# Performance work log

Hardware: AMD Instinct MI355X
Metric: run time of the kernel (lower is better)

Reference implementation:

```python
import jax, jax.numpy as jnp
import numpy as np

EPS_LN = 1e-5
EPS_STD = 1e-5


def _ln_dim1(z, g, b):
    # LayerNorm over channel dim (axis=1) of (B, C, T) or (B, C, 1)
    mu = z.mean(axis=1, keepdims=True)
    var = ((z - mu) ** 2).mean(axis=1, keepdims=True)
    return (z - mu) * jax.lax.rsqrt(var + EPS_LN) * g[None, :, None] + b[None, :, None]


def _stats(x, m):
    # weighted mean/std over time axis; m broadcasts over channels
    mean = (m * x).sum(axis=2)                                   # (B, C)
    std = jnp.sqrt(jnp.maximum((m * x * x).sum(axis=2) - mean ** 2, EPS_STD))
    return mean, std


def setup_inputs() -> dict:
    key = jax.random.key(0)
    ks = jax.random.split(key, 4)
    B, C, T, H = 16, 1536, 2000, 128
    x = jax.random.normal(ks[0], (B, C, T), dtype=jnp.float32)
    mask = jnp.ones((B, 1, T), dtype=jnp.float32)
    # attention MLP params (conv1x1 -> relu -> LN(dim=1) -> tanh -> conv1x1)
    w1 = jax.random.normal(ks[1], (H, 3 * C), dtype=jnp.float32) * (1.0 / np.sqrt(3 * C))
    b1 = jnp.zeros((H,), jnp.float32)
    g1 = jnp.ones((H,), jnp.float32)
    be1 = jnp.zeros((H,), jnp.float32)
    w2 = jax.random.normal(ks[2], (C, H), dtype=jnp.float32) * (1.0 / np.sqrt(H))
    b2 = jnp.zeros((C,), jnp.float32)
    g2 = jnp.ones((2 * C,), jnp.float32)
    be2 = jnp.zeros((2 * C,), jnp.float32)
    return {"x": x, "mask": mask, "w1": w1, "b1": b1, "g1": g1, "be1": be1,
            "w2": w2, "b2": b2, "g2": g2, "be2": be2}


def reference(x, mask, w1, b1, g1, be1, w2, b2, g2, be2):
    B, C, T = x.shape
    # time_attention: append masked global mean/std, broadcast over T
    total = mask.sum(axis=2, keepdims=True)                      # (B,1,1)
    mean0, std0 = _stats(x, mask / total)                        # (B,C)
    x_in = jnp.concatenate([
        x,
        jnp.broadcast_to(mean0[:, :, None], (B, C, T)),
        jnp.broadcast_to(std0[:, :, None], (B, C, T)),
    ], axis=1)                                                   # (B,3C,T)
    # attention MLP (conv1x1 == channel matmul)
    h = jnp.einsum("hc,bct->bht", w1, x_in) + b1[None, :, None]  # (B,H,T)
    h = jnp.tanh(_ln_dim1(jax.nn.relu(h), g1, be1))
    alpha = jnp.einsum("ch,bht->bct", w2, h) + b2[None, :, None]  # (B,C,T)
    # masked softmax over time
    alpha = jnp.where(mask == 0, -jnp.inf, alpha)
    alpha = jax.nn.softmax(alpha, axis=2)
    # attention-weighted stats
    mean, std = _stats(x, alpha)                                 # (B,C) each
    out = jnp.concatenate([mean, std], axis=1)[:, :, None]       # (B,2C,1)
    return _ln_dim1(out, g2, be2)
```

## Files before the change

kernel.cpp:

```cpp
#include <hip/hip_runtime.h>
#include <math.h>

constexpr int B_  = 16;
constexpr int C_  = 1536;
constexpr int T_  = 2000;
constexpr int H_  = 128;
constexpr int C3_ = 3 * C_;
constexpr int C2_ = 2 * C_;
constexpr int NT_ = 4;

typedef short bf8 __attribute__((ext_vector_type(8)));
typedef short bf4 __attribute__((ext_vector_type(4)));
typedef float f4  __attribute__((ext_vector_type(4)));

__device__ inline unsigned short f2b(float f) {
  unsigned int u = __builtin_bit_cast(unsigned int, f);
  unsigned int r = (u + 0x7FFFu + ((u >> 16) & 1u)) >> 16;
  return (unsigned short)r;
}

__global__ __launch_bounds__(256) void k_stats(
    const float* __restrict__ x, const float* __restrict__ mask,
    float* __restrict__ mean0, float* __restrict__ std0) {
  const int wave = threadIdx.x >> 6;
  const int lane = threadIdx.x & 63;
  const int row = blockIdx.x * 4 + wave;
  const int b = row / C_;
  const float4* xr = (const float4*)(x + (size_t)row * T_);
  const float4* mr = (const float4*)(mask + (size_t)b * T_);
  float sm = 0.f, s1 = 0.f, s2 = 0.f;
  for (int i = lane; i < T_ / 4; i += 64) {
    float4 xv = xr[i];
    float4 mv = mr[i];
    sm += mv.x + mv.y + mv.z + mv.w;
    s1 += mv.x * xv.x + mv.y * xv.y + mv.z * xv.z + mv.w * xv.w;
    s2 += mv.x * xv.x * xv.x + mv.y * xv.y * xv.y + mv.z * xv.z * xv.z + mv.w * xv.w * xv.w;
  }
#pragma unroll
  for (int off = 32; off; off >>= 1) {
    sm += __shfl_xor(sm, off);
    s1 += __shfl_xor(s1, off);
    s2 += __shfl_xor(s2, off);
  }
  if (lane == 0) {
    float mean = s1 / sm;
    float var = s2 / sm - mean * mean;
    mean0[row] = mean;
    std0[row] = sqrtf(fmaxf(var, 1e-5f));
  }
}

__global__ __launch_bounds__(256) void k_hconst_wl1(
    const float* __restrict__ w1, const float* __restrict__ b1,
    const float* __restrict__ mean0, const float* __restrict__ std0,
    const float* __restrict__ w2,
    float* __restrict__ hconst, float* __restrict__ wl1) {
  const int wave = threadIdx.x >> 6;
  const int lane = threadIdx.x & 63;
  if (blockIdx.x < B_ * H_ / 4) {
    const int idx = blockIdx.x * 4 + wave;
    const int b = idx >> 7;
    const int h = idx & (H_ - 1);
    const float* wm  = w1 + (size_t)h * C3_ + C_;
    const float* wsd = wm + C_;
    const float* mn = mean0 + b * C_;
    const float* sd = std0 + b * C_;
    float s = 0.f;
    for (int c = lane; c < C_; c += 64)
      s += wm[c] * mn[c] + wsd[c] * sd[c];
#pragma unroll
    for (int off = 32; off; off >>= 1) s += __shfl_xor(s, off);
    if (lane == 0) hconst[idx] = s + b1[h];
  } else {
    const int c = (blockIdx.x - B_ * H_ / 4) * 4 + wave;
    const float* wr = w2 + (size_t)c * H_;
    float s = fabsf(wr[lane]) + fabsf(wr[lane + 64]);
#pragma unroll
    for (int off = 32; off; off >>= 1) s += __shfl_xor(s, off);
    if (lane == 0) wl1[c] = s;
  }
}

__global__ __launch_bounds__(256) void k_gemm1_ln(
    const float* __restrict__ x, const float* __restrict__ w1,
    const float* __restrict__ hconst, const float* __restrict__ g1,
    const float* __restrict__ be1, unsigned short* __restrict__ hlnT) {
  __shared__ __align__(16) short As[2][128 * 32];
  __shared__ __align__(16) short Bs[2][64 * 32];
  const int b = blockIdx.y;
  const int t0 = blockIdx.x * 64;
  const int tid = threadIdx.x;
  const int lane = tid & 63;
  const int w = tid >> 6;
  const int l15 = lane & 15;
  const int l4 = lane >> 4;

  float4 va[4], vb[2];

  f4 acc[8];
#pragma unroll
  for (int mi = 0; mi < 8; ++mi) { f4 z = {0.f, 0.f, 0.f, 0.f}; acc[mi] = z; }

#define G1_GLOAD(K0)                                                          \
  {                                                                           \
    _Pragma("unroll")                                                         \
    for (int q = 0; q < 4; ++q) {                                             \
      int idx = q * 256 + tid;                                                \
      int row = idx >> 3, j4 = idx & 7;                                       \
      va[q] = *(const float4*)(w1 + (size_t)row * C3_ + (K0) + j4 * 4);       \
    }                                                                         \
    _Pragma("unroll")                                                         \
    for (int q = 0; q < 2; ++q) {                                             \
      int idx = q * 256 + tid;                                                \
      int k = idx >> 4, t4 = idx & 15;                                        \
      int t = t0 + t4 * 4;                                                    \
      if (t < T_)                                                             \
        vb[q] = *(const float4*)(x + ((size_t)(b * C_ + (K0) + k)) * T_ + t); \
      else                                                                    \
        vb[q] = make_float4(0.f, 0.f, 0.f, 0.f);                              \
    }                                                                         \
  }
#define G1_LSTORE(BUF)                                                        \
  {                                                                           \
    _Pragma("unroll")                                                         \
    for (int q = 0; q < 4; ++q) {                                             \
      int idx = q * 256 + tid;                                                \
      int row = idx >> 3, j4 = idx & 7;                                       \
      int slot = (j4 >> 1) ^ ((row >> 2) & 3);                                \
      bf4 p;                                                                  \
      p[0] = (short)f2b(va[q].x); p[1] = (short)f2b(va[q].y);                 \
      p[2] = (short)f2b(va[q].z); p[3] = (short)f2b(va[q].w);                 \
      *(bf4*)&As[BUF][row * 32 + slot * 8 + (j4 & 1) * 4] = p;                \
    }                                                                         \
    _Pragma("unroll")                                                         \
    for (int q = 0; q < 2; ++q) {                                             \
      int idx = q * 256 + tid;                                                \
      int k = idx >> 4, t4 = idx & 15;                                        \
      float vv[4] = {vb[q].x, vb[q].y, vb[q].z, vb[q].w};                     \
      _Pragma("unroll")                                                       \
      for (int j = 0; j < 4; ++j) {                                           \
        int row = t4 * 4 + j;                                                 \
        int slot = (k >> 3) ^ ((row >> 2) & 3);                               \
        Bs[BUF][row * 32 + slot * 8 + (k & 7)] = (short)f2b(vv[j]);           \
      }                                                                       \
    }                                                                         \
  }

  G1_GLOAD(0);
  G1_LSTORE(0);
  __syncthreads();

  const int fA = (l15 >> 2) & 3;
  const int NS = C_ / 32;
  for (int s = 0; s < NS; ++s) {
    const int cur = s & 1;
    if (s + 1 < NS) G1_GLOAD((s + 1) * 32);
    {
      const int browB = w * 16 + l15;
      bf8 bfr = *(const bf8*)&Bs[cur][browB * 32 + (l4 ^ fA) * 8];
#pragma unroll
      for (int mi = 0; mi < 8; ++mi) {
        bf8 afr = *(const bf8*)&As[cur][(mi * 16 + l15) * 32 + (l4 ^ fA) * 8];
        acc[mi] = __builtin_amdgcn_mfma_f32_16x16x32_bf16(afr, bfr, acc[mi], 0, 0, 0);
      }
    }
    if (s + 1 < NS) G1_LSTORE(cur ^ 1);
    __syncthreads();
  }

  const int t = t0 + w * 16 + l15;
  float sum = 0.f, ssq = 0.f;
#pragma unroll
  for (int mi = 0; mi < 8; ++mi) {
    float4 h4 = *(const float4*)(hconst + b * H_ + mi * 16 + l4 * 4);
    const float* hp = (const float*)&h4;
#pragma unroll
    for (int reg = 0; reg < 4; ++reg) {
      float v = fmaxf(acc[mi][reg] + hp[reg], 0.f);
      acc[mi][reg] = v;
      sum += v;
      ssq += v * v;
    }
  }
  sum += __shfl_xor(sum, 16); sum += __shfl_xor(sum, 32);
  ssq += __shfl_xor(ssq, 16); ssq += __shfl_xor(ssq, 32);
  const float mean = sum * (1.f / 128.f);
  const float rstd = rsqrtf(ssq * (1.f / 128.f) - mean * mean + 1e-5f);
  if (t < T_) {
    unsigned short* dst = hlnT + ((size_t)b * T_ + t) * H_;
#pragma unroll
    for (int mi = 0; mi < 8; ++mi) {
      float4 g4 = *(const float4*)(g1 + mi * 16 + l4 * 4);
      float4 e4 = *(const float4*)(be1 + mi * 16 + l4 * 4);
      const float* gp = (const float*)&g4;
      const float* ep = (const float*)&e4;
      bf4 p;
#pragma unroll
      for (int reg = 0; reg < 4; ++reg) {
        float o = tanhf((acc[mi][reg] - mean) * rstd * gp[reg] + ep[reg]);
        p[reg] = (short)f2b(o);
      }
      *(bf4*)&dst[mi * 16 + l4 * 4] = p;
    }
  }
}

__global__ __launch_bounds__(256) void k_gemm2_pool(
    const float* __restrict__ x, const float* __restrict__ mask,
    const float* __restrict__ w2, const unsigned short* __restrict__ hlnT,
    const float* __restrict__ wl1,
    float* __restrict__ ps0, float* __restrict__ ps1, float* __restrict__ ps2) {
  __shared__ __align__(16) short Hs[2][64 * 128];
  const int b = blockIdx.y;
  const int c0 = blockIdx.x * 128;
  const int part = blockIdx.z;
  const int tb = part * 512;
  const int te = min(tb + 512, T_);
  const int tid = threadIdx.x;
  const int lane = tid & 63;
  const int w = tid >> 6;
  const int l15 = lane & 15;
  const int l4 = lane >> 4;

  bf8 af[2][4];
#pragma unroll
  for (int mi = 0; mi < 2; ++mi)
#pragma unroll
    for (int ks = 0; ks < 4; ++ks) {
      const float* src = w2 + (size_t)(c0 + w * 32 + mi * 16 + l15) * H_ + (ks * 4 + l4) * 8;
      float4 v0 = *(const float4*)src;
      float4 v1 = *(const float4*)(src + 4);
      bf8 p;
      p[0] = (short)f2b(v0.x); p[1] = (short)f2b(v0.y);
      p[2] = (short)f2b(v0.z); p[3] = (short)f2b(v0.w);
      p[4] = (short)f2b(v1.x); p[5] = (short)f2b(v1.y);
      p[6] = (short)f2b(v1.z); p[7] = (short)f2b(v1.w);
      af[mi][ks] = p;
    }

  float Mc[8];
#pragma unroll
  for (int mi = 0; mi < 2; ++mi) {
    float4 m4 = *(const float4*)(wl1 + c0 + w * 32 + mi * 16 + l4 * 4);
    Mc[mi * 4 + 0] = m4.x; Mc[mi * 4 + 1] = m4.y;
    Mc[mi * 4 + 2] = m4.z; Mc[mi * 4 + 3] = m4.w;
  }

  float s0[8], s1[8], s2[8];
#pragma unroll
  for (int r = 0; r < 8; ++r) { s0[r] = 0.f; s1[r] = 0.f; s2[r] = 0.f; }

  bf8 hreg[4];
#define G2_HLOAD(T0)                                                          \
  {                                                                           \
    _Pragma("unroll")                                                         \
    for (int q = 0; q < 4; ++q) {                                             \
      int idx = q * 256 + tid;                                                \
      int row = idx >> 4, slot = idx & 15;                                    \
      int t = (T0) + row;                                                     \
      if (t > T_ - 1) t = T_ - 1;                                             \
      hreg[q] = *(const bf8*)(hlnT + ((size_t)b * T_ + t) * H_ + slot * 8);   \
    }                                                                         \
  }
#define G2_HSTORE(BUF)                                                        \
  {                                                                           \
    _Pragma("unroll")                                                         \
    for (int q = 0; q < 4; ++q) {                                             \
      int idx = q * 256 + tid;                                                \
      int row = idx >> 4, slot = idx & 15;                                    \
      *(bf8*)&Hs[BUF][row * 128 + (slot ^ (row & 15)) * 8] = hreg[q];         \
    }                                                                         \
  }

  G2_HLOAD(tb);
  G2_HSTORE(0);
  __syncthreads();

  const int NCH = (te - tb + 63) / 64;
  for (int ch = 0; ch < NCH; ++ch) {
    const int t0 = tb + ch * 64;
    const int cur = ch & 1;
    if (ch + 1 < NCH) G2_HLOAD(t0 + 64);

    float mk[4];
    int tcol[4];
#pragma unroll
    for (int nj = 0; nj < 4; ++nj) {
      int t = t0 + nj * 16 + l15;
      tcol[nj] = (t < T_) ? t : (T_ - 1);
      mk[nj] = (t < T_) ? mask[(size_t)b * T_ + t] : 0.f;
    }
    float xv[8][4];
#pragma unroll
    for (int mi = 0; mi < 2; ++mi)
#pragma unroll
      for (int reg = 0; reg < 4; ++reg) {
        const int c = c0 + w * 32 + mi * 16 + l4 * 4 + reg;
        const float* xrow = x + ((size_t)(b * C_ + c)) * T_;
#pragma unroll
        for (int nj = 0; nj < 4; ++nj) xv[mi * 4 + reg][nj] = xrow[tcol[nj]];
      }

    f4 acc[2][4];
#pragma unroll
    for (int mi = 0; mi < 2; ++mi)
#pragma unroll
      for (int nj = 0; nj < 4; ++nj) { f4 z = {0.f, 0.f, 0.f, 0.f}; acc[mi][nj] = z; }

#pragma unroll
    for (int ks = 0; ks < 4; ++ks) {
      const int sw = (ks * 4 + l4) ^ l15;
      bf8 bb[4];
#pragma unroll
      for (int nj = 0; nj < 4; ++nj)
        bb[nj] = *(const bf8*)&Hs[cur][(nj * 16 + l15) * 128 + sw * 8];
#pragma unroll
      for (int nj = 0; nj < 4; ++nj) {
        acc[0][nj] = __builtin_amdgcn_mfma_f32_16x16x32_bf16(af[0][ks], bb[nj], acc[0][nj], 0, 0, 0);
        acc[1][nj] = __builtin_amdgcn_mfma_f32_16x16x32_bf16(af[1][ks], bb[nj], acc[1][nj], 0, 0, 0);
      }
    }

#pragma unroll
    for (int mi = 0; mi < 2; ++mi)
#pragma unroll
      for (int reg = 0; reg < 4; ++reg) {
        const int r = mi * 4 + reg;
        float a0 = s0[r], a1 = s1[r], a2 = s2[r];
#pragma unroll
        for (int nj = 0; nj < 4; ++nj) {
          float e = (mk[nj] != 0.f) ? __expf(acc[mi][nj][reg] - Mc[r]) : 0.f;
          float xvv = xv[r][nj];
          a0 += e; a1 += e * xvv; a2 += e * xvv * xvv;
        }
        s0[r] = a0; s1[r] = a1; s2[r] = a2;
      }

    if (ch + 1 < NCH) G2_HSTORE(cur ^ 1);
    __syncthreads();
  }

#pragma unroll
  for (int off = 1; off < 16; off <<= 1) {
#pragma unroll
    for (int r = 0; r < 8; ++r) {
      s0[r] += __shfl_xor(s0[r], off);
      s1[r] += __shfl_xor(s1[r], off);
      s2[r] += __shfl_xor(s2[r], off);
    }
  }
  if (l15 == 0) {
#pragma unroll
    for (int mi = 0; mi < 2; ++mi)
#pragma unroll
      for (int reg = 0; reg < 4; ++reg) {
        const int r = mi * 4 + reg;
        const int c = c0 + w * 32 + mi * 16 + l4 * 4 + reg;
        const size_t j = ((size_t)(b * NT_ + part)) * C_ + c;
        ps0[j] = s0[r]; ps1[j] = s1[r]; ps2[j] = s2[r];
      }
  }
}

__global__ __launch_bounds__(256) void k_pool_merge(
    const float* __restrict__ ps0, const float* __restrict__ ps1,
    const float* __restrict__ ps2, float* __restrict__ pooled) {
  const int idx = blockIdx.x * 256 + threadIdx.x;
  const int b = idx / C_;
  const int c = idx - b * C_;
  float s0 = 0.f, s1 = 0.f, s2 = 0.f;
#pragma unroll
  for (int p = 0; p < NT_; ++p) {
    const size_t j = ((size_t)(b * NT_ + p)) * C_ + c;
    s0 += ps0[j]; s1 += ps1[j]; s2 += ps2[j];
  }
  float mean = s1 / s0;
  float var = s2 / s0 - mean * mean;
  pooled[b * C2_ + c] = mean;
  pooled[b * C2_ + C_ + c] = sqrtf(fmaxf(var, 1e-5f));
}

__global__ __launch_bounds__(256) void k_final_ln(
    const float* __restrict__ pooled, const float* __restrict__ g2,
    const float* __restrict__ be2, float* __restrict__ out) {
  __shared__ float rs[8];
  const int b = blockIdx.x;
  const int tid = threadIdx.x;
  const int lane = tid & 63;
  const int wave = tid >> 6;
  const float* p = pooled + b * C2_;
  float s = 0.f, q = 0.f;
  for (int i = tid; i < C2_; i += 256) {
    float v = p[i];
    s += v;
    q += v * v;
  }
#pragma unroll
  for (int off = 32; off; off >>= 1) {
    s += __shfl_xor(s, off);
    q += __shfl_xor(q, off);
  }
  if (lane == 0) { rs[wave] = s; rs[4 + wave] = q; }
  __syncthreads();
  s = rs[0] + rs[1] + rs[2] + rs[3];
  q = rs[4] + rs[5] + rs[6] + rs[7];
  float mean = s * (1.f / C2_);
  float var = q * (1.f / C2_) - mean * mean;
  float rstd = rsqrtf(var + 1e-5f);
  for (int i = tid; i < C2_; i += 256)
    out[b * C2_ + i] = (p[i] - mean) * rstd * g2[i] + be2[i];
}

extern "C" void kernel_launch(void* const* d_in, const int* in_sizes, int n_in,
                              void* d_out, int out_size, void* d_ws, size_t ws_size,
                              hipStream_t stream) {
  const float* x    = (const float*)d_in[0];
  const float* mask = (const float*)d_in[1];
  const float* w1   = (const float*)d_in[2];
  const float* b1   = (const float*)d_in[3];
  const float* g1   = (const float*)d_in[4];
  const float* be1  = (const float*)d_in[5];
  const float* w2   = (const float*)d_in[6];
  const float* g2   = (const float*)d_in[8];
  const float* be2  = (const float*)d_in[9];
  float* out = (float*)d_out;

  float* ws     = (float*)d_ws;
  float* mean0  = ws;
  float* std0   = mean0 + B_ * C_;
  float* hconst = std0 + B_ * C_;
  float* pooled = hconst + B_ * H_;
  float* wl1    = pooled + B_ * C2_;
  float* ps0    = wl1 + C_;
  float* ps1    = ps0 + B_ * NT_ * C_;
  float* ps2    = ps1 + B_ * NT_ * C_;
  unsigned short* hlnT = (unsigned short*)(ps2 + B_ * NT_ * C_);

  k_stats<<<dim3(B_ * C_ / 4), dim3(256), 0, stream>>>(x, mask, mean0, std0);
  k_hconst_wl1<<<dim3(B_ * H_ / 4 + C_ / 4), dim3(256), 0, stream>>>(
      w1, b1, mean0, std0, w2, hconst, wl1);
  k_gemm1_ln<<<dim3((T_ + 63) / 64, B_), dim3(256), 0, stream>>>(x, w1, hconst, g1, be1, hlnT);
  k_gemm2_pool<<<dim3(C_ / 128, B_, NT_), dim3(256), 0, stream>>>(x, mask, w2, hlnT, wl1,
                                                                  ps0, ps1, ps2);
  k_pool_merge<<<dim3(B_ * C_ / 256), dim3(256), 0, stream>>>(ps0, ps1, ps2, pooled);
  k_final_ln<<<dim3(B_), dim3(256), 0, stream>>>(pooled, g2, be2, out);
}
```

Before: 164.2 us.

## Fuse masked mean/std statistics pass into GEMM1 and split off LayerNorm epilogue

The standalone statistics kernel that re-read all of x is removed. Per-tile masked sums of x and x^2 are now computed inside the first GEMM while its x tiles are loaded, and a small reduce kernel merges them. Because hconst depends on those stats, GEMM1 writes the pre-activation h to an fp32 buffer, and a separate epilogue kernel adds hconst and applies relu, LayerNorm and tanh. This saves one full pass over x (about 200 MB) at the cost of an extra h_pre round trip (about 16 MB), partial-sum buffers and one more kernel launch.

```diff
diff --git a/kernel.cpp b/kernel.cpp
--- a/kernel.cpp
+++ b/kernel.cpp
@@ -8,6 +8,7 @@
 constexpr int C3_ = 3 * C_;
 constexpr int C2_ = 2 * C_;
 constexpr int NT_ = 4;
+constexpr int NTL_ = 32;
 
 typedef short bf8 __attribute__((ext_vector_type(8)));
 typedef short bf4 __attribute__((ext_vector_type(4)));
@@ -19,35 +20,171 @@
   return (unsigned short)r;
 }
 
-__global__ __launch_bounds__(256) void k_stats(
-    const float* __restrict__ x, const float* __restrict__ mask,
+__global__ __launch_bounds__(256) void k_gemm1_stats(
+    const float* __restrict__ x, const float* __restrict__ w1,
+    const float* __restrict__ mask,
+    float* __restrict__ h_pre, float* __restrict__ sp1, float* __restrict__ sp2) {
+  __shared__ __align__(16) short As[2][128 * 32];
+  __shared__ __align__(16) short Bs[2][64 * 32];
+  const int b = blockIdx.y;
+  const int tile = blockIdx.x;
+  const int t0 = tile * 64;
+  const int tid = threadIdx.x;
+  const int lane = tid & 63;
+  const int w = tid >> 6;
+  const int l15 = lane & 15;
+  const int l4 = lane >> 4;
+
+  float4 va[4], vb[2];
+
+  const int t4 = tid & 15;
+  float mreg[4];
+#pragma unroll
+  for (int j = 0; j < 4; ++j) {
+    int t = t0 + t4 * 4 + j;
+    mreg[j] = (t < T_) ? mask[(size_t)b * T_ + t] : 0.f;
+  }
+  float* sp1row = sp1 + ((size_t)b * NTL_ + tile) * C_;
+  float* sp2row = sp2 + ((size_t)b * NTL_ + tile) * C_;
+
+  f4 acc[8];
+#pragma unroll
+  for (int mi = 0; mi < 8; ++mi) { f4 z = {0.f, 0.f, 0.f, 0.f}; acc[mi] = z; }
+
+#define G1_GLOAD(K0)                                                          \
+  {                                                                           \
+    _Pragma("unroll")                                                         \
+    for (int q = 0; q < 4; ++q) {                                             \
+      int idx = q * 256 + tid;                                                \
+      int row = idx >> 3, j4 = idx & 7;                                       \
+      va[q] = *(const float4*)(w1 + (size_t)row * C3_ + (K0) + j4 * 4);       \
+    }                                                                         \
+    _Pragma("unroll")                                                         \
+    for (int q = 0; q < 2; ++q) {                                             \
+      int idx = q * 256 + tid;                                                \
+      int k = idx >> 4;                                                       \
+      int t = t0 + t4 * 4;                                                    \
+      if (t < T_)                                                             \
+        vb[q] = *(const float4*)(x + ((size_t)(b * C_ + (K0) + k)) * T_ + t); \
+      else                                                                    \
+        vb[q] = make_float4(0.f, 0.f, 0.f, 0.f);                              \
+    }                                                                         \
+  }
+#define G1_LSTORE(BUF)                                                        \
+  {                                                                           \
+    _Pragma("unroll")                                                         \
+    for (int q = 0; q < 4; ++q) {                                             \
+      int idx = q * 256 + tid;                                                \
+      int row = idx >> 3, j4 = idx & 7;                                       \
+      int slot = (j4 >> 1) ^ ((row >> 2) & 3);                                \
+      bf4 p;                                                                  \
+      p[0] = (short)f2b(va[q].x); p[1] = (short)f2b(va[q].y);                 \
+      p[2] = (short)f2b(va[q].z); p[3] = (short)f2b(va[q].w);                 \
+      *(bf4*)&As[BUF][row * 32 + slot * 8 + (j4 & 1) * 4] = p;                \
+    }                                                                         \
+    _Pragma("unroll")                                                         \
+    for (int q = 0; q < 2; ++q) {                                             \
+      int idx = q * 256 + tid;                                                \
+      int k = idx >> 4;                                                       \
+      float vv[4] = {vb[q].x, vb[q].y, vb[q].z, vb[q].w};                     \
+      _Pragma("unroll")                                                       \
+      for (int j = 0; j < 4; ++j) {                                           \
+        int row = t4 * 4 + j;                                                 \
+        int slot = (k >> 3) ^ ((row >> 2) & 3);                               \
+        Bs[BUF][row * 32 + slot * 8 + (k & 7)] = (short)f2b(vv[j]);           \
+      }                                                                       \
+    }                                                                         \
+  }
+#define G1_STATS(K0)                                                          \
+  {                                                                           \
+    _Pragma("unroll")                                                         \
+    for (int q = 0; q < 2; ++q) {                                             \
+      float vv[4] = {vb[q].x, vb[q].y, vb[q].z, vb[q].w};                     \
+      float a1 = 0.f, a2 = 0.f;                                               \
+      _Pragma("unroll")                                                       \
+      for (int j = 0; j < 4; ++j) {                                           \
+        float mx = mreg[j] * vv[j];                                           \
+        a1 += mx;                                                             \
+        a2 = fmaf(mx, vv[j], a2);                                             \
+      }                                                                       \
+      _Pragma("unroll")                                                       \
+      for (int off = 1; off < 16; off <<= 1) {                                \
+        a1 += __shfl_xor(a1, off);                                            \
+        a2 += __shfl_xor(a2, off);                                            \
+      }                                                                       \
+      if (t4 == 0) {                                                          \
+        int c = (K0) + q * 16 + (tid >> 4);                                   \
+        sp1row[c] = a1;                                                       \
+        sp2row[c] = a2;                                                       \
+      }                                                                       \
+    }                                                                         \
+  }
+
+  G1_GLOAD(0);
+  G1_LSTORE(0);
+  G1_STATS(0);
+  __syncthreads();
+
+  const int fA = (l15 >> 2) & 3;
+  const int NS = C_ / 32;
+  for (int s = 0; s < NS; ++s) {
+    const int cur = s & 1;
+    if (s + 1 < NS) G1_GLOAD((s + 1) * 32);
+    {
+      const int browB = w * 16 + l15;
+      bf8 bfr = *(const bf8*)&Bs[cur][browB * 32 + (l4 ^ fA) * 8];
+#pragma unroll
+      for (int mi = 0; mi < 8; ++mi) {
+        bf8 afr = *(const bf8*)&As[cur][(mi * 16 + l15) * 32 + (l4 ^ fA) * 8];
+        acc[mi] = __builtin_amdgcn_mfma_f32_16x16x32_bf16(afr, bfr, acc[mi], 0, 0, 0);
+      }
+    }
+    if (s + 1 < NS) {
+      G1_LSTORE(cur ^ 1);
+      G1_STATS((s + 1) * 32);
+    }
+    __syncthreads();
+  }
+
+  const int t = t0 + w * 16 + l15;
+  if (t < T_) {
+    float* dst = h_pre + ((size_t)b * T_ + t) * H_;
+#pragma unroll
+    for (int mi = 0; mi < 8; ++mi)
+      *(f4*)&dst[mi * 16 + l4 * 4] = acc[mi];
+  }
+}
+
+__global__ __launch_bounds__(256) void k_stats_reduce(
+    const float* __restrict__ sp1, const float* __restrict__ sp2,
+    const float* __restrict__ mask,
     float* __restrict__ mean0, float* __restrict__ std0) {
-  const int wave = threadIdx.x >> 6;
-  const int lane = threadIdx.x & 63;
-  const int row = blockIdx.x * 4 + wave;
-  const int b = row / C_;
-  const float4* xr = (const float4*)(x + (size_t)row * T_);
-  const float4* mr = (const float4*)(mask + (size_t)b * T_);
-  float sm = 0.f, s1 = 0.f, s2 = 0.f;
-  for (int i = lane; i < T_ / 4; i += 64) {
-    float4 xv = xr[i];
-    float4 mv = mr[i];
-    sm += mv.x + mv.y + mv.z + mv.w;
-    s1 += mv.x * xv.x + mv.y * xv.y + mv.z * xv.z + mv.w * xv.w;
-    s2 += mv.x * xv.x * xv.x + mv.y * xv.y * xv.y + mv.z * xv.z * xv.z + mv.w * xv.w * xv.w;
-  }
-#pragma unroll
-  for (int off = 32; off; off >>= 1) {
-    sm += __shfl_xor(sm, off);
-    s1 += __shfl_xor(s1, off);
-    s2 += __shfl_xor(s2, off);
-  }
-  if (lane == 0) {
-    float mean = s1 / sm;
-    float var = s2 / sm - mean * mean;
-    mean0[row] = mean;
-    std0[row] = sqrtf(fmaxf(var, 1e-5f));
-  }
+  __shared__ float rs[4];
+  const int b = blockIdx.x / (C_ / 256);
+  const int chunk = blockIdx.x % (C_ / 256);
+  const int tid = threadIdx.x;
+  const int lane = tid & 63;
+  const int wv = tid >> 6;
+  float sm = 0.f;
+  for (int i = tid; i < T_; i += 256) sm += mask[(size_t)b * T_ + i];
+#pragma unroll
+  for (int off = 32; off; off >>= 1) sm += __shfl_xor(sm, off);
+  if (lane == 0) rs[wv] = sm;
+  __syncthreads();
+  sm = rs[0] + rs[1] + rs[2] + rs[3];
+
+  const int c = chunk * 256 + tid;
+  float s1 = 0.f, s2 = 0.f;
+#pragma unroll 8
+  for (int tile = 0; tile < NTL_; ++tile) {
+    const size_t j = ((size_t)b * NTL_ + tile) * C_ + c;
+    s1 += sp1[j];
+    s2 += sp2[j];
+  }
+  float mean = s1 / sm;
+  float var = s2 / sm - mean * mean;
+  mean0[b * C_ + c] = mean;
+  std0[b * C_ + c] = sqrtf(fmaxf(var, 1e-5f));
 }
 
 __global__ __launch_bounds__(256) void k_hconst_wl1(
@@ -81,127 +218,48 @@
   }
 }
 
-__global__ __launch_bounds__(256) void k_gemm1_ln(
-    const float* __restrict__ x, const float* __restrict__ w1,
-    const float* __restrict__ hconst, const float* __restrict__ g1,
-    const float* __restrict__ be1, unsigned short* __restrict__ hlnT) {
-  __shared__ __align__(16) short As[2][128 * 32];
-  __shared__ __align__(16) short Bs[2][64 * 32];
+__global__ __launch_bounds__(256) void k_ln_epi(
+    const float* __restrict__ h_pre, const float* __restrict__ hconst,
+    const float* __restrict__ g1, const float* __restrict__ be1,
+    unsigned short* __restrict__ hlnT) {
   const int b = blockIdx.y;
-  const int t0 = blockIdx.x * 64;
-  const int tid = threadIdx.x;
-  const int lane = tid & 63;
-  const int w = tid >> 6;
-  const int l15 = lane & 15;
-  const int l4 = lane >> 4;
-
-  float4 va[4], vb[2];
-
-  f4 acc[8];
-#pragma unroll
-  for (int mi = 0; mi < 8; ++mi) { f4 z = {0.f, 0.f, 0.f, 0.f}; acc[mi] = z; }
-
-#define G1_GLOAD(K0)                                                          \
-  {                                                                           \
-    _Pragma("unroll")                                                         \
-    for (int q = 0; q < 4; ++q) {                                             \
-      int idx = q * 256 + tid;                                                \
-      int row = idx >> 3, j4 = idx & 7;                                       \
-      va[q] = *(const float4*)(w1 + (size_t)row * C3_ + (K0) + j4 * 4);       \
-    }                                                                         \
-    _Pragma("unroll")                                                         \
-    for (int q = 0; q < 2; ++q) {                                             \
-      int idx = q * 256 + tid;                                                \
-      int k = idx >> 4, t4 = idx & 15;                                        \
-      int t = t0 + t4 * 4;                                                    \
-      if (t < T_)                                                             \
-        vb[q] = *(const float4*)(x + ((size_t)(b * C_ + (K0) + k)) * T_ + t); \
-      else                                                                    \
-        vb[q] = make_float4(0.f, 0.f, 0.f, 0.f);                              \
-    }                                                                         \
-  }
-#define G1_LSTORE(BUF)                                                        \
-  {                                                                           \
-    _Pragma("unroll")                                                         \
-    for (int q = 0; q < 4; ++q) {                                             \
-      int idx = q * 256 + tid;                                                \
-      int row = idx >> 3, j4 = idx & 7;                                       \
-      int slot = (j4 >> 1) ^ ((row >> 2) & 3);                                \
-      bf4 p;                                                                  \
-      p[0] = (short)f2b(va[q].x); p[1] = (short)f2b(va[q].y);                 \
-      p[2] = (short)f2b(va[q].z); p[3] = (short)f2b(va[q].w);                 \
-      *(bf4*)&As[BUF][row * 32 + slot * 8 + (j4 & 1) * 4] = p;                \
-    }                                                                         \
-    _Pragma("unroll")                                                         \
-    for (int q = 0; q < 2; ++q) {                                             \
-      int idx = q * 256 + tid;                                                \
-      int k = idx >> 4, t4 = idx & 15;                                        \
-      float vv[4] = {vb[q].x, vb[q].y, vb[q].z, vb[q].w};                     \
-      _Pragma("unroll")                                                       \
-      for (int j = 0; j < 4; ++j) {                                           \
-        int row = t4 * 4 + j;                                                 \
-        int slot = (k >> 3) ^ ((row >> 2) & 3);                               \
-        Bs[BUF][row * 32 + slot * 8 + (k & 7)] = (short)f2b(vv[j]);           \
-      }                                                                       \
-    }                                                                         \
-  }
-
-  G1_GLOAD(0);
-  G1_LSTORE(0);
-  __syncthreads();
-
-  const int fA = (l15 >> 2) & 3;
-  const int NS = C_ / 32;
-  for (int s = 0; s < NS; ++s) {
-    const int cur = s & 1;
-    if (s + 1 < NS) G1_GLOAD((s + 1) * 32);
-    {
-      const int browB = w * 16 + l15;
-      bf8 bfr = *(const bf8*)&Bs[cur][browB * 32 + (l4 ^ fA) * 8];
-#pragma unroll
-      for (int mi = 0; mi < 8; ++mi) {
-        bf8 afr = *(const bf8*)&As[cur][(mi * 16 + l15) * 32 + (l4 ^ fA) * 8];
-        acc[mi] = __builtin_amdgcn_mfma_f32_16x16x32_bf16(afr, bfr, acc[mi], 0, 0, 0);
-      }
-    }
-    if (s + 1 < NS) G1_LSTORE(cur ^ 1);
-    __syncthreads();
-  }
-
-  const int t = t0 + w * 16 + l15;
+  const int t = blockIdx.x * 64 + (threadIdx.x >> 2);
+  const int part = threadIdx.x & 3;
+  if (t >= T_) return;
+  const float* src = h_pre + ((size_t)b * T_ + t) * H_ + part * 32;
+  const float* hc = hconst + b * H_ + part * 32;
+  float v[32];
   float sum = 0.f, ssq = 0.f;
 #pragma unroll
-  for (int mi = 0; mi < 8; ++mi) {
-    float4 h4 = *(const float4*)(hconst + b * H_ + mi * 16 + l4 * 4);
+  for (int j = 0; j < 8; ++j) {
+    float4 h4 = *(const float4*)(src + j * 4);
+    float4 c4 = *(const float4*)(hc + j * 4);
     const float* hp = (const float*)&h4;
-#pragma unroll
-    for (int reg = 0; reg < 4; ++reg) {
-      float v = fmaxf(acc[mi][reg] + hp[reg], 0.f);
-      acc[mi][reg] = v;
-      sum += v;
-      ssq += v * v;
-    }
-  }
-  sum += __shfl_xor(sum, 16); sum += __shfl_xor(sum, 32);
-  ssq += __shfl_xor(ssq, 16); ssq += __shfl_xor(ssq, 32);
+    const float* cp = (const float*)&c4;
+#pragma unroll
+    for (int r = 0; r < 4; ++r) {
+      float u = fmaxf(hp[r] + cp[r], 0.f);
+      v[j * 4 + r] = u;
+      sum += u;
+      ssq += u * u;
+    }
+  }
+  sum += __shfl_xor(sum, 1); sum += __shfl_xor(sum, 2);
+  ssq += __shfl_xor(ssq, 1); ssq += __shfl_xor(ssq, 2);
   const float mean = sum * (1.f / 128.f);
   const float rstd = rsqrtf(ssq * (1.f / 128.f) - mean * mean + 1e-5f);
-  if (t < T_) {
-    unsigned short* dst = hlnT + ((size_t)b * T_ + t) * H_;
-#pragma unroll
-    for (int mi = 0; mi < 8; ++mi) {
-      float4 g4 = *(const float4*)(g1 + mi * 16 + l4 * 4);
-      float4 e4 = *(const float4*)(be1 + mi * 16 + l4 * 4);
-      const float* gp = (const float*)&g4;
-      const float* ep = (const float*)&e4;
-      bf4 p;
-#pragma unroll
-      for (int reg = 0; reg < 4; ++reg) {
-        float o = tanhf((acc[mi][reg] - mean) * rstd * gp[reg] + ep[reg]);
-        p[reg] = (short)f2b(o);
-      }
-      *(bf4*)&dst[mi * 16 + l4 * 4] = p;
-    }
+  unsigned short* dst = hlnT + ((size_t)b * T_ + t) * H_ + part * 32;
+  const float* gp = g1 + part * 32;
+  const float* ep = be1 + part * 32;
+#pragma unroll
+  for (int m = 0; m < 4; ++m) {
+    bf8 p;
+#pragma unroll
+    for (int r = 0; r < 8; ++r) {
+      int j = m * 8 + r;
+      p[r] = (short)f2b(tanhf((v[j] - mean) * rstd * gp[j] + ep[j]));
+    }
+    *(bf8*)&dst[m * 8] = p;
   }
 }
 
@@ -434,12 +492,16 @@
   float* ps0    = wl1 + C_;
   float* ps1    = ps0 + B_ * NT_ * C_;
   float* ps2    = ps1 + B_ * NT_ * C_;
-  unsigned short* hlnT = (unsigned short*)(ps2 + B_ * NT_ * C_);
-
-  k_stats<<<dim3(B_ * C_ / 4), dim3(256), 0, stream>>>(x, mask, mean0, std0);
+  float* sp1    = ps2 + B_ * NT_ * C_;
+  float* sp2    = sp1 + B_ * NTL_ * C_;
+  float* h_pre  = sp2 + B_ * NTL_ * C_;
+  unsigned short* hlnT = (unsigned short*)(h_pre + (size_t)B_ * T_ * H_);
+
+  k_gemm1_stats<<<dim3(NTL_, B_), dim3(256), 0, stream>>>(x, w1, mask, h_pre, sp1, sp2);
+  k_stats_reduce<<<dim3(B_ * C_ / 256), dim3(256), 0, stream>>>(sp1, sp2, mask, mean0, std0);
   k_hconst_wl1<<<dim3(B_ * H_ / 4 + C_ / 4), dim3(256), 0, stream>>>(
       w1, b1, mean0, std0, w2, hconst, wl1);
-  k_gemm1_ln<<<dim3((T_ + 63) / 64, B_), dim3(256), 0, stream>>>(x, w1, hconst, g1, be1, hlnT);
+  k_ln_epi<<<dim3(NTL_, B_), dim3(256), 0, stream>>>(h_pre, hconst, g1, be1, hlnT);
   k_gemm2_pool<<<dim3(C_ / 128, B_, NT_), dim3(256), 0, stream>>>(x, mask, w2, hlnT, wl1,
                                                                   ps0, ps1, ps2);
   k_pool_merge<<<dim3(B_ * C_ / 256), dim3(256), 0, stream>>>(ps0, ps1, ps2, pooled);
```

After: 163.8 us. No clear change (-0.2%).

## Load x fragments directly into registers in gemm1, halve gemm2 channel tile

Applied to the files above, without the earlier changes.

In the first GEMM, the x operand is no longer staged through shared memory. Each lane loads its own 8 strided x values per k-step straight into registers, with a two-register ping-pong, and converts them to bf16 for the MFMA B fragment. This drops the Bs LDS buffer and its scattered 2-byte stores. The pooling GEMM now uses 64-channel blocks instead of 128, which doubles the grid and cuts per-thread registers. The bf16 conversion now uses the compiler's native __bf16 cast. The tradeoff is uncoalesced-looking global loads, since each lane reads 8 rows with stride T, though lanes in a row are contiguous in t.

```diff
diff --git a/kernel.cpp b/kernel.cpp
--- a/kernel.cpp
+++ b/kernel.cpp
@@ -1,4 +1,5 @@
 #include <hip/hip_runtime.h>
+#include <hip/hip_bf16.h>
 #include <math.h>
 
 constexpr int B_  = 16;
@@ -14,9 +15,8 @@
 typedef float f4  __attribute__((ext_vector_type(4)));
 
 __device__ inline unsigned short f2b(float f) {
-  unsigned int u = __builtin_bit_cast(unsigned int, f);
-  unsigned int r = (u + 0x7FFFu + ((u >> 16) & 1u)) >> 16;
-  return (unsigned short)r;
+  __bf16 h = (__bf16)f;
+  return __builtin_bit_cast(unsigned short, h);
 }
 
 __global__ __launch_bounds__(256) void k_stats(
@@ -86,7 +86,6 @@
     const float* __restrict__ hconst, const float* __restrict__ g1,
     const float* __restrict__ be1, unsigned short* __restrict__ hlnT) {
   __shared__ __align__(16) short As[2][128 * 32];
-  __shared__ __align__(16) short Bs[2][64 * 32];
   const int b = blockIdx.y;
   const int t0 = blockIdx.x * 64;
   const int tid = threadIdx.x;
@@ -94,14 +93,17 @@
   const int w = tid >> 6;
   const int l15 = lane & 15;
   const int l4 = lane >> 4;
-
-  float4 va[4], vb[2];
+  const int tcl = min(t0 + w * 16 + l15, T_ - 1);
+  const float* xcol = x + (size_t)b * C_ * T_ + tcl;
+
+  float4 va[4];
+  float xs0[8], xs1[8];
 
   f4 acc[8];
 #pragma unroll
   for (int mi = 0; mi < 8; ++mi) { f4 z = {0.f, 0.f, 0.f, 0.f}; acc[mi] = z; }
 
-#define G1_GLOAD(K0)                                                          \
+#define G1_GLOADA(K0)                                                         \
   {                                                                           \
     _Pragma("unroll")                                                         \
     for (int q = 0; q < 4; ++q) {                                             \
@@ -109,18 +111,14 @@
       int row = idx >> 3, j4 = idx & 7;                                       \
       va[q] = *(const float4*)(w1 + (size_t)row * C3_ + (K0) + j4 * 4);       \
     }                                                                         \
-    _Pragma("unroll")                                                         \
-    for (int q = 0; q < 2; ++q) {                                             \
-      int idx = q * 256 + tid;                                                \
-      int k = idx >> 4, t4 = idx & 15;                                        \
-      int t = t0 + t4 * 4;                                                    \
-      if (t < T_)                                                             \
-        vb[q] = *(const float4*)(x + ((size_t)(b * C_ + (K0) + k)) * T_ + t); \
-      else                                                                    \
-        vb[q] = make_float4(0.f, 0.f, 0.f, 0.f);                              \
-    }                                                                         \
-  }
-#define G1_LSTORE(BUF)                                                        \
+  }
+#define G1_GLOADB(K0, XS)                                                     \
+  {                                                                           \
+    const float* xb = xcol + ((size_t)(K0) + l4 * 8) * T_;                    \
+    _Pragma("unroll")                                                         \
+    for (int j = 0; j < 8; ++j) XS[j] = xb[(size_t)j * T_];                   \
+  }
+#define G1_LSTOREA(BUF)                                                       \
   {                                                                           \
     _Pragma("unroll")                                                         \
     for (int q = 0; q < 4; ++q) {                                             \
@@ -132,40 +130,36 @@
       p[2] = (short)f2b(va[q].z); p[3] = (short)f2b(va[q].w);                 \
       *(bf4*)&As[BUF][row * 32 + slot * 8 + (j4 & 1) * 4] = p;                \
     }                                                                         \
-    _Pragma("unroll")                                                         \
-    for (int q = 0; q < 2; ++q) {                                             \
-      int idx = q * 256 + tid;                                                \
-      int k = idx >> 4, t4 = idx & 15;                                        \
-      float vv[4] = {vb[q].x, vb[q].y, vb[q].z, vb[q].w};                     \
-      _Pragma("unroll")                                                       \
-      for (int j = 0; j < 4; ++j) {                                           \
-        int row = t4 * 4 + j;                                                 \
-        int slot = (k >> 3) ^ ((row >> 2) & 3);                               \
-        Bs[BUF][row * 32 + slot * 8 + (k & 7)] = (short)f2b(vv[j]);           \
-      }                                                                       \
-    }                                                                         \
-  }
-
-  G1_GLOAD(0);
-  G1_LSTORE(0);
-  __syncthreads();
+  }
+#define G1_STEP(S, XSCUR, XSNXT, CUR)                                         \
+  {                                                                           \
+    if ((S) + 1 < NS) {                                                       \
+      G1_GLOADA(((S) + 1) * 32);                                              \
+      G1_GLOADB(((S) + 1) * 32, XSNXT);                                       \
+    }                                                                         \
+    bf8 bfr;                                                                  \
+    _Pragma("unroll")                                                         \
+    for (int j = 0; j < 8; ++j) bfr[j] = (short)f2b(XSCUR[j]);                \
+    _Pragma("unroll")                                                         \
+    for (int mi = 0; mi < 8; ++mi) {                                          \
+      bf8 afr = *(const bf8*)&As[CUR][(mi * 16 + l15) * 32 + (l4 ^ fA) * 8];  \
+      acc[mi] = __builtin_amdgcn_mfma_f32_16x16x32_bf16(afr, bfr, acc[mi], 0, 0, 0); \
+    }                                                                         \
+    if ((S) + 1 < NS) G1_LSTOREA(CUR ^ 1);                                    \
+    __syncthreads();                                                          \
+  }
 
   const int fA = (l15 >> 2) & 3;
   const int NS = C_ / 32;
-  for (int s = 0; s < NS; ++s) {
-    const int cur = s & 1;
-    if (s + 1 < NS) G1_GLOAD((s + 1) * 32);
-    {
-      const int browB = w * 16 + l15;
-      bf8 bfr = *(const bf8*)&Bs[cur][browB * 32 + (l4 ^ fA) * 8];
-#pragma unroll
-      for (int mi = 0; mi < 8; ++mi) {
-        bf8 afr = *(const bf8*)&As[cur][(mi * 16 + l15) * 32 + (l4 ^ fA) * 8];
-        acc[mi] = __builtin_amdgcn_mfma_f32_16x16x32_bf16(afr, bfr, acc[mi], 0, 0, 0);
-      }
-    }
-    if (s + 1 < NS) G1_LSTORE(cur ^ 1);
-    __syncthreads();
+
+  G1_GLOADA(0);
+  G1_GLOADB(0, xs0);
+  G1_LSTOREA(0);
+  __syncthreads();
+
+  for (int sp = 0; sp < NS / 2; ++sp) {
+    G1_STEP(2 * sp,     xs0, xs1, 0);
+    G1_STEP(2 * sp + 1, xs1, xs0, 1);
   }
 
   const int t = t0 + w * 16 + l15;
@@ -212,7 +206,7 @@
     float* __restrict__ ps0, float* __restrict__ ps1, float* __restrict__ ps2) {
   __shared__ __align__(16) short Hs[2][64 * 128];
   const int b = blockIdx.y;
-  const int c0 = blockIdx.x * 128;
+  const int c0 = blockIdx.x * 64;
   const int part = blockIdx.z;
   const int tb = part * 512;
   const int te = min(tb + 512, T_);
@@ -222,33 +216,29 @@
   const int l15 = lane & 15;
   const int l4 = lane >> 4;
 
-  bf8 af[2][4];
-#pragma unroll
-  for (int mi = 0; mi < 2; ++mi)
-#pragma unroll
-    for (int ks = 0; ks < 4; ++ks) {
-      const float* src = w2 + (size_t)(c0 + w * 32 + mi * 16 + l15) * H_ + (ks * 4 + l4) * 8;
-      float4 v0 = *(const float4*)src;
-      float4 v1 = *(const float4*)(src + 4);
-      bf8 p;
-      p[0] = (short)f2b(v0.x); p[1] = (short)f2b(v0.y);
-      p[2] = (short)f2b(v0.z); p[3] = (short)f2b(v0.w);
-      p[4] = (short)f2b(v1.x); p[5] = (short)f2b(v1.y);
-      p[6] = (short)f2b(v1.z); p[7] = (short)f2b(v1.w);
-      af[mi][ks] = p;
-    }
-
-  float Mc[8];
-#pragma unroll
-  for (int mi = 0; mi < 2; ++mi) {
-    float4 m4 = *(const float4*)(wl1 + c0 + w * 32 + mi * 16 + l4 * 4);
-    Mc[mi * 4 + 0] = m4.x; Mc[mi * 4 + 1] = m4.y;
-    Mc[mi * 4 + 2] = m4.z; Mc[mi * 4 + 3] = m4.w;
-  }
-
-  float s0[8], s1[8], s2[8];
-#pragma unroll
-  for (int r = 0; r < 8; ++r) { s0[r] = 0.f; s1[r] = 0.f; s2[r] = 0.f; }
+  bf8 af[4];
+#pragma unroll
+  for (int ks = 0; ks < 4; ++ks) {
+    const float* src = w2 + (size_t)(c0 + w * 16 + l15) * H_ + (ks * 4 + l4) * 8;
+    float4 v0 = *(const float4*)src;
+    float4 v1 = *(const float4*)(src + 4);
+    bf8 p;
+    p[0] = (short)f2b(v0.x); p[1] = (short)f2b(v0.y);
+    p[2] = (short)f2b(v0.z); p[3] = (short)f2b(v0.w);
+    p[4] = (short)f2b(v1.x); p[5] = (short)f2b(v1.y);
+    p[6] = (short)f2b(v1.z); p[7] = (short)f2b(v1.w);
+    af[ks] = p;
+  }
+
+  float Mc[4];
+  {
+    float4 m4 = *(const float4*)(wl1 + c0 + w * 16 + l4 * 4);
+    Mc[0] = m4.x; Mc[1] = m4.y; Mc[2] = m4.z; Mc[3] = m4.w;
+  }
+
+  float s0[4], s1[4], s2[4];
+#pragma unroll
+  for (int r = 0; r < 4; ++r) { s0[r] = 0.f; s1[r] = 0.f; s2[r] = 0.f; }
 
   bf8 hreg[4];
 #define G2_HLOAD(T0)                                                          \
@@ -290,22 +280,18 @@
       tcol[nj] = (t < T_) ? t : (T_ - 1);
       mk[nj] = (t < T_) ? mask[(size_t)b * T_ + t] : 0.f;
     }
-    float xv[8][4];
-#pragma unroll
-    for (int mi = 0; mi < 2; ++mi)
-#pragma unroll
-      for (int reg = 0; reg < 4; ++reg) {
-        const int c = c0 + w * 32 + mi * 16 + l4 * 4 + reg;
-        const float* xrow = x + ((size_t)(b * C_ + c)) * T_;
-#pragma unroll
-        for (int nj = 0; nj < 4; ++nj) xv[mi * 4 + reg][nj] = xrow[tcol[nj]];
-      }
-
-    f4 acc[2][4];
-#pragma unroll
-    for (int mi = 0; mi < 2; ++mi)
-#pragma unroll
-      for (int nj = 0; nj < 4; ++nj) { f4 z = {0.f, 0.f, 0.f, 0.f}; acc[mi][nj] = z; }
+    float xv[4][4];
+#pragma unroll
+    for (int reg = 0; reg < 4; ++reg) {
+      const int c = c0 + w * 16 + l4 * 4 + reg;
+      const float* xrow = x + ((size_t)(b * C_ + c)) * T_;
+#pragma unroll
+      for (int nj = 0; nj < 4; ++nj) xv[reg][nj] = xrow[tcol[nj]];
+    }
+
+    f4 acc[4];
+#pragma unroll
+    for (int nj = 0; nj < 4; ++nj) { f4 z = {0.f, 0.f, 0.f, 0.f}; acc[nj] = z; }
 
 #pragma unroll
     for (int ks = 0; ks < 4; ++ks) {
@@ -315,26 +301,21 @@
       for (int nj = 0; nj < 4; ++nj)
         bb[nj] = *(const bf8*)&Hs[cur][(nj * 16 + l15) * 128 + sw * 8];
 #pragma unroll
+      for (int nj = 0; nj < 4; ++nj)
+        acc[nj] = __builtin_amdgcn_mfma_f32_16x16x32_bf16(af[ks], bb[nj], acc[nj], 0, 0, 0);
+    }
+
+#pragma unroll
+    for (int reg = 0; reg < 4; ++reg) {
+      float a0 = s0[reg], a1 = s1[reg], a2 = s2[reg];
+#pragma unroll
       for (int nj = 0; nj < 4; ++nj) {
-        acc[0][nj] = __builtin_amdgcn_mfma_f32_16x16x32_bf16(af[0][ks], bb[nj], acc[0][nj], 0, 0, 0);
-        acc[1][nj] = __builtin_amdgcn_mfma_f32_16x16x32_bf16(af[1][ks], bb[nj], acc[1][nj], 0, 0, 0);
+        float e = (mk[nj] != 0.f) ? __expf(acc[nj][reg] - Mc[reg]) : 0.f;
+        float xvv = xv[reg][nj];
+        a0 += e; a1 += e * xvv; a2 += e * xvv * xvv;
       }
-    }
-
-#pragma unroll
-    for (int mi = 0; mi < 2; ++mi)
-#pragma unroll
-      for (int reg = 0; reg < 4; ++reg) {
-        const int r = mi * 4 + reg;
-        float a0 = s0[r], a1 = s1[r], a2 = s2[r];
-#pragma unroll
-        for (int nj = 0; nj < 4; ++nj) {
-          float e = (mk[nj] != 0.f) ? __expf(acc[mi][nj][reg] - Mc[r]) : 0.f;
-          float xvv = xv[r][nj];
-          a0 += e; a1 += e * xvv; a2 += e * xvv * xvv;
-        }
-        s0[r] = a0; s1[r] = a1; s2[r] = a2;
-      }
+      s0[reg] = a0; s1[reg] = a1; s2[reg] = a2;
+    }
 
     if (ch + 1 < NCH) G2_HSTORE(cur ^ 1);
     __syncthreads();
@@ -343,7 +324,7 @@
 #pragma unroll
   for (int off = 1; off < 16; off <<= 1) {
 #pragma unroll
-    for (int r = 0; r < 8; ++r) {
+    for (int r = 0; r < 4; ++r) {
       s0[r] += __shfl_xor(s0[r], off);
       s1[r] += __shfl_xor(s1[r], off);
       s2[r] += __shfl_xor(s2[r], off);
@@ -351,14 +332,11 @@
   }
   if (l15 == 0) {
 #pragma unroll
-    for (int mi = 0; mi < 2; ++mi)
-#pragma unroll
-      for (int reg = 0; reg < 4; ++reg) {
-        const int r = mi * 4 + reg;
-        const int c = c0 + w * 32 + mi * 16 + l4 * 4 + reg;
-        const size_t j = ((size_t)(b * NT_ + part)) * C_ + c;
-        ps0[j] = s0[r]; ps1[j] = s1[r]; ps2[j] = s2[r];
-      }
+    for (int reg = 0; reg < 4; ++reg) {
+      const int c = c0 + w * 16 + l4 * 4 + reg;
+      const size_t j = ((size_t)(b * NT_ + part)) * C_ + c;
+      ps0[j] = s0[reg]; ps1[j] = s1[reg]; ps2[j] = s2[reg];
+    }
   }
 }
 
@@ -440,8 +418,8 @@
   k_hconst_wl1<<<dim3(B_ * H_ / 4 + C_ / 4), dim3(256), 0, stream>>>(
       w1, b1, mean0, std0, w2, hconst, wl1);
   k_gemm1_ln<<<dim3((T_ + 63) / 64, B_), dim3(256), 0, stream>>>(x, w1, hconst, g1, be1, hlnT);
-  k_gemm2_pool<<<dim3(C_ / 128, B_, NT_), dim3(256), 0, stream>>>(x, mask, w2, hlnT, wl1,
-                                                                  ps0, ps1, ps2);
+  k_gemm2_pool<<<dim3(C_ / 64, B_, NT_), dim3(256), 0, stream>>>(x, mask, w2, hlnT, wl1,
+                                                                 ps0, ps1, ps2);
   k_pool_merge<<<dim3(B_ * C_ / 256), dim3(256), 0, stream>>>(ps0, ps1, ps2, pooled);
   k_final_ln<<<dim3(B_), dim3(256), 0, stream>>>(pooled, g2, be2, out);
 }
```

Measured after the change: 150.1 us. 8.6% less time.
